# Kernel optimization log

Measured on AMD Instinct MI355X. Metric: run time of the kernel, lower is better.

The kernel has to match this reference:

```python
import jax, jax.numpy as jnp
import numpy as np

# RVQECell configuration (matches init_kwargs)
I_SZ, W_SZ, STAGES, ORDER, DEGREE = 6, 12, 3, 2, 2
BIAS = float(np.pi / 2)
ANC = ORDER - 1                      # ancillas_for_order(order) = order - 1
N = I_SZ + W_SZ + ANC                # 19 qubits
B = 32
INOUT = list(range(I_SZ))            # lanes 0..5
WORK = list(range(I_SZ, I_SZ + W_SZ))  # lanes 6..17
C_CTRL = I_SZ + W_SZ - 1             # controls per neuron = 17


def setup_inputs() -> dict:
    key = jax.random.key(0)
    ks = jax.random.split(key, 9)
    s = 0.1  # small init keeps neuron angles in a well-conditioned range
    psi = jax.random.normal(ks[0], (B, 2 ** N), jnp.float32)
    psi = psi / jnp.linalg.norm(psi, axis=1, keepdims=True)  # normalized kets
    return {
        "batch": psi,
        "w_in1": jax.random.normal(ks[1], (W_SZ, C_CTRL), jnp.float32) * s,
        "w_in2": jax.random.normal(ks[2], (W_SZ, C_CTRL, C_CTRL), jnp.float32) * s,
        "w_u": jax.random.normal(ks[3], (STAGES, W_SZ), jnp.float32) * s,
        "w_k1": jax.random.normal(ks[4], (STAGES, W_SZ, C_CTRL), jnp.float32) * s,
        "w_k2": jax.random.normal(ks[5], (STAGES, W_SZ, C_CTRL, C_CTRL), jnp.float32) * s,
        "w_out1": jax.random.normal(ks[6], (I_SZ, C_CTRL), jnp.float32) * s,
        "w_out2": jax.random.normal(ks[7], (I_SZ, C_CTRL, C_CTRL), jnp.float32) * s,
        "inputs": jax.random.randint(ks[8], (B, I_SZ), 0, 2, dtype=jnp.int32),
    }


def _rot_y(state, lane, alpha):
    # real rotation [[cos a, -sin a], [sin a, cos a]] on qubit `lane`.
    ax = lane + 1  # +1 for batch axis; state shape [B] + [2]*N
    c, s = jnp.cos(alpha), jnp.sin(alpha)
    p0 = jax.lax.index_in_dim(state, 0, ax, keepdims=True)
    p1 = jax.lax.index_in_dim(state, 1, ax, keepdims=True)
    return jnp.concatenate([c * p0 - s * p1, s * p0 + c * p1], axis=ax)


def _neuron(state, outlane, th1, th2):
    # Fast (deterministic RUS) quantum neuron of given ORDER/DEGREE:
    # per control-basis-branch rotation of `outlane` by alpha(x),
    # phi(x) = bias + sum_i th1_i x_i + sum_{i<j} th2_ij x_i x_j (degree 2),
    # alpha = q^(order-1)(phi), q(t) = arctan(tan(t)^2), stable via arctan2.
    controls = [l for l in range(I_SZ + W_SZ) if l != outlane]
    Cn = len(controls)
    x = jnp.arange(2 ** Cn)
    shifts = jnp.arange(Cn - 1, -1, -1)
    bits = ((x[:, None] >> shifts[None, :]) & 1).astype(state.dtype)  # [2^Cn, Cn]
    phi = BIAS + bits @ th1
    if DEGREE >= 2:
        phi = phi + jnp.einsum('xi,ij,xj->x', bits, jnp.triu(th2, 1), bits)
    alpha = phi
    for _ in range(ORDER - 1):
        alpha = jnp.arctan2(jnp.sin(alpha) ** 2, jnp.cos(alpha) ** 2)
    shape = [1] + [2 if l in controls else 1 for l in range(N)]
    return _rot_y(state, outlane, alpha.reshape(shape))


def _bitflip(state_flat, inputs):
    # Vectorized batched BitFlipLayer: X on inout lane i where inputs[b,i]==1,
    # i.e. permute amplitudes by XOR of the flip mask (lane 0 most significant).
    shifts = (N - 1) - jnp.arange(I_SZ)
    f = jnp.sum(inputs.astype(jnp.int32) << shifts[None, :], axis=1)  # [B]
    idx = jnp.arange(2 ** N, dtype=jnp.int32)[None, :] ^ f[:, None]
    return jnp.take_along_axis(state_flat, idx, axis=1)


def reference(batch, w_in1, w_in2, w_u, w_k1, w_k2, w_out1, w_out2, inputs):
    psi = _bitflip(batch, inputs).reshape((B,) + (2,) * N)
    # input layer: one neuron per workspace lane
    for j, out in enumerate(WORK):
        psi = _neuron(psi, out, w_in1[j], w_in2[j])
    # kernel layer: stages x (UnitaryLayer(workspace) + neurons)
    for st in range(STAGES):
        for j, lane in enumerate(WORK):
            psi = _rot_y(psi, lane, w_u[st, j])
        for j, out in enumerate(WORK):
            psi = _neuron(psi, out, w_k1[st, j], w_k2[st, j])
    psi = _bitflip(psi.reshape(B, -1), inputs).reshape((B,) + (2,) * N)
    # output layer: one neuron per inout lane
    for j, out in enumerate(INOUT):
        psi = _neuron(psi, out, w_out1[j], w_out2[j])
    # measurement probabilities over inout lanes: marginal of |amp|^2
    probs = jnp.sum(psi ** 2, axis=tuple(range(1 + I_SZ, 1 + N))).reshape(B, -1)
    return probs, psi.reshape(B, -1)
```

## Files before the change

kernel.cpp:

```cpp
#include <hip/hip_runtime.h>
#include <math.h>


#define BIAS_F 1.57079632679489662f

typedef float v4f __attribute__((ext_vector_type(4)));

__device__ __forceinline__ float4 ntload4(const float* p) {
    v4f v = __builtin_nontemporal_load((const v4f*)p);
    return make_float4(v.x, v.y, v.z, v.w);
}
__device__ __forceinline__ void ntstore4(float* p, float4 f) {
    v4f v = {f.x, f.y, f.z, f.w};
    __builtin_nontemporal_store(v, (v4f*)p);
}

__device__ __forceinline__ int SW(int i) { return i ^ ((i >> 3) & 0x1C); }
__device__ __forceinline__ float4 ldsld4(const float* st, int i) {
    return *(const float4*)&st[SW(i)];
}
__device__ __forceinline__ void ldsst4(float* st, int i, float4 v) {
    *(float4*)&st[SW(i)] = v;
}

__device__ __forceinline__ float2 dec(float v) {
    float t = sqrtf(fmaf(-v, v, 1.0f));
    float c = v >= 0.f ? v : t;
    float s = v >= 0.f ? t : -v;
    return make_float2(c, s);
}
__device__ __forceinline__ float4 dec4(float2 g) {
    float2 u = dec(g.x), w = dec(g.y);
    return make_float4(u.x, u.y, w.x, w.y);
}
#define LD2(p) (*(const float2*)(p))
#define LD4(p) (*(const float4*)(p))

__device__ __forceinline__ void rot4(float4& A, float4& B, float4 e) {
    float ax = A.x, ay = A.y, az = A.z, aw = A.w;
    A.x = e.x * ax - e.y * B.x;  B.x = e.y * ax + e.x * B.x;
    A.y = e.x * ay - e.y * B.y;  B.y = e.y * ay + e.x * B.y;
    A.z = e.z * az - e.w * B.z;  B.z = e.w * az + e.z * B.z;
    A.w = e.z * aw - e.w * B.w;  B.w = e.w * aw + e.z * B.w;
}
__device__ __forceinline__ void rotq(float4& P, float c, float s) {
    float px = P.x, py = P.y;
    P.x = c * px - s * P.z;  P.z = s * px + c * P.z;
    P.y = c * py - s * P.w;  P.w = s * py + c * P.w;
}

__global__ __launch_bounds__(256) void tables_kernel(
    const float* __restrict__ w_in1, const float* __restrict__ w_in2,
    const float* __restrict__ w_k1,  const float* __restrict__ w_k2,
    const float* __restrict__ w_out1, const float* __restrict__ w_out2,
    float* __restrict__ tab)
{
    const int n = blockIdx.y;
    const int hi = blockIdx.x;
    const int tid = threadIdx.x;
    const float* th1;
    const float* th2;
    if (n < 12)      { th1 = w_in1 + n * 17;         th2 = w_in2 + n * 289; }
    else if (n < 48) { th1 = w_k1 + (n - 12) * 17;   th2 = w_k2 + (n - 12) * 289; }
    else             { th1 = w_out1 + (n - 48) * 17; th2 = w_out2 + (n - 48) * 289; }

    float bu[9], bt[8];
#pragma unroll
    for (int i = 0; i < 9; ++i) bu[i] = (float)((hi >> (8 - i)) & 1);
#pragma unroll
    for (int j = 0; j < 8; ++j) bt[j] = (float)((tid >> (7 - j)) & 1);

    float phi = BIAS_F;
#pragma unroll
    for (int i = 0; i < 9; ++i) {
        float acc = th1[i];
#pragma unroll
        for (int j = i + 1; j < 9; ++j) acc += bu[j] * th2[i * 17 + j];
#pragma unroll
        for (int j = 0; j < 8; ++j)     acc += bt[j] * th2[i * 17 + 9 + j];
        phi += bu[i] * acc;
    }
#pragma unroll
    for (int a = 0; a < 8; ++a) {
        float acc = th1[9 + a];
#pragma unroll
        for (int b2 = a + 1; b2 < 8; ++b2) acc += bt[b2] * th2[(9 + a) * 17 + 9 + b2];
        phi += bt[a] * acc;
    }
    float sp, cp;
    sincosf(phi, &sp, &cp);
    float c2 = cp * cp, s2 = sp * sp;
    float d = c2 * c2 + s2 * s2;
    float r = rsqrtf(d);
    r = r * (1.5f - 0.5f * d * r * r);
    float ca = c2 * r, sa = s2 * r;
    tab[(size_t)n * 131072 + ((hi << 8) | tid)] = (ca <= sa) ? ca : -sa;
}

template <int PA, bool NEUR>
__device__ __forceinline__ void pass_hi2(float* l0, float* l1, int t8,
    const float* tA, const float* tB, const float* tC,
    float cA, float sA, float cB, float sB, float cC, float sC)
{
    const int lowb = PA - 4;
    const int low = t8 & ((1 << lowb) - 1);
    const int high = t8 >> lowb;
    const int i0 = (high << (PA + 1)) | (low << 2);
    const int x0 = (high << (PA - 1)) | (low << 1);
    const int oa = 1 << PA, ob = oa >> 1, oc = oa >> 2;
    const int dhi = oa >> 2, dlo = oa >> 3;
    float2 pa0, pa1, pa2, pa3, pb0, pb1, pb2, pb3, pc0, pc1, pc2, pc3;
    if (NEUR) {
        pa0 = LD2(&tA[x0]);       pa1 = LD2(&tA[x0 + dlo]);
        pa2 = LD2(&tA[x0 + dhi]); pa3 = LD2(&tA[x0 + dhi + dlo]);
        pb0 = LD2(&tB[x0]);       pb1 = LD2(&tB[x0 + dlo]);
        pb2 = LD2(&tB[x0 + dhi]); pb3 = LD2(&tB[x0 + dhi + dlo]);
        pc0 = LD2(&tC[x0]);       pc1 = LD2(&tC[x0 + dlo]);
        pc2 = LD2(&tC[x0 + dhi]); pc3 = LD2(&tC[x0 + dhi + dlo]);
    }
#pragma unroll
    for (int s = 0; s < 2; ++s) {
        float* sl = (s == 0) ? l0 : l1;
        float4 Q000 = ldsld4(sl, i0),            Q001 = ldsld4(sl, i0 + oc);
        float4 Q010 = ldsld4(sl, i0 + ob),       Q011 = ldsld4(sl, i0 + ob + oc);
        float4 Q100 = ldsld4(sl, i0 + oa),       Q101 = ldsld4(sl, i0 + oa + oc);
        float4 Q110 = ldsld4(sl, i0 + oa + ob),  Q111 = ldsld4(sl, i0 + oa + ob + oc);
        if (NEUR) {
            {
                float4 e00 = dec4(pa0), e01 = dec4(pa1), e10 = dec4(pa2), e11 = dec4(pa3);
                rot4(Q000, Q100, e00); rot4(Q001, Q101, e01);
                rot4(Q010, Q110, e10); rot4(Q011, Q111, e11);
            }
            {
                float4 e00 = dec4(pb0), e01 = dec4(pb1), e10 = dec4(pb2), e11 = dec4(pb3);
                rot4(Q000, Q010, e00); rot4(Q001, Q011, e01);
                rot4(Q100, Q110, e10); rot4(Q101, Q111, e11);
            }
            {
                float4 e00 = dec4(pc0), e01 = dec4(pc1), e10 = dec4(pc2), e11 = dec4(pc3);
                rot4(Q000, Q001, e00); rot4(Q010, Q011, e01);
                rot4(Q100, Q101, e10); rot4(Q110, Q111, e11);
            }
        } else {
            float4 eA = make_float4(cA, sA, cA, sA);
            rot4(Q000, Q100, eA); rot4(Q001, Q101, eA);
            rot4(Q010, Q110, eA); rot4(Q011, Q111, eA);
            float4 eB = make_float4(cB, sB, cB, sB);
            rot4(Q000, Q010, eB); rot4(Q001, Q011, eB);
            rot4(Q100, Q110, eB); rot4(Q101, Q111, eB);
            float4 eC = make_float4(cC, sC, cC, sC);
            rot4(Q000, Q001, eC); rot4(Q010, Q011, eC);
            rot4(Q100, Q101, eC); rot4(Q110, Q111, eC);
        }
        ldsst4(sl, i0, Q000);            ldsst4(sl, i0 + oc, Q001);
        ldsst4(sl, i0 + ob, Q010);       ldsst4(sl, i0 + ob + oc, Q011);
        ldsst4(sl, i0 + oa, Q100);       ldsst4(sl, i0 + oa + oc, Q101);
        ldsst4(sl, i0 + oa + ob, Q110);  ldsst4(sl, i0 + oa + ob + oc, Q111);
    }
}

template <bool NEUR>
__device__ __forceinline__ void pass_lo2(float* l0, float* l1, int t8,
    const float* tA, const float* tB, const float* tC,
    float cA, float sA, float cB, float sB, float cC, float sC)
{
    const int i0 = t8 << 5, x0 = t8 << 3;
    float4 qa0, qa1, qb0, qb1, qc0, qc1;
    if (NEUR) {
        qa0 = LD4(&tA[x0]); qa1 = LD4(&tA[x0 + 4]);
        qb0 = LD4(&tB[x0]); qb1 = LD4(&tB[x0 + 4]);
        qc0 = LD4(&tC[x0]); qc1 = LD4(&tC[x0 + 4]);
    }
#pragma unroll
    for (int s = 0; s < 2; ++s) {
        float* sl = (s == 0) ? l0 : l1;
        float4 Q0 = ldsld4(sl, i0),      Q1 = ldsld4(sl, i0 + 4);
        float4 Q2 = ldsld4(sl, i0 + 8),  Q3 = ldsld4(sl, i0 + 12);
        float4 Q4 = ldsld4(sl, i0 + 16), Q5 = ldsld4(sl, i0 + 20);
        float4 Q6 = ldsld4(sl, i0 + 24), Q7 = ldsld4(sl, i0 + 28);
        if (NEUR) {
            rot4(Q0, Q2, dec4(make_float2(qa0.x, qa0.y)));
            rot4(Q1, Q3, dec4(make_float2(qa0.z, qa0.w)));
            rot4(Q4, Q6, dec4(make_float2(qa1.x, qa1.y)));
            rot4(Q5, Q7, dec4(make_float2(qa1.z, qa1.w)));
            rot4(Q0, Q1, dec4(make_float2(qb0.x, qb0.y)));
            rot4(Q2, Q3, dec4(make_float2(qb0.z, qb0.w)));
            rot4(Q4, Q5, dec4(make_float2(qb1.x, qb1.y)));
            rot4(Q6, Q7, dec4(make_float2(qb1.z, qb1.w)));
            { float2 d = dec(qc0.x); rotq(Q0, d.x, d.y); }
            { float2 d = dec(qc0.y); rotq(Q1, d.x, d.y); }
            { float2 d = dec(qc0.z); rotq(Q2, d.x, d.y); }
            { float2 d = dec(qc0.w); rotq(Q3, d.x, d.y); }
            { float2 d = dec(qc1.x); rotq(Q4, d.x, d.y); }
            { float2 d = dec(qc1.y); rotq(Q5, d.x, d.y); }
            { float2 d = dec(qc1.z); rotq(Q6, d.x, d.y); }
            { float2 d = dec(qc1.w); rotq(Q7, d.x, d.y); }
        } else {
            float4 eA = make_float4(cA, sA, cA, sA);
            rot4(Q0, Q2, eA); rot4(Q1, Q3, eA); rot4(Q4, Q6, eA); rot4(Q5, Q7, eA);
            float4 eB = make_float4(cB, sB, cB, sB);
            rot4(Q0, Q1, eB); rot4(Q2, Q3, eB); rot4(Q4, Q5, eB); rot4(Q6, Q7, eB);
            rotq(Q0, cC, sC); rotq(Q1, cC, sC); rotq(Q2, cC, sC); rotq(Q3, cC, sC);
            rotq(Q4, cC, sC); rotq(Q5, cC, sC); rotq(Q6, cC, sC); rotq(Q7, cC, sC);
        }
        ldsst4(sl, i0, Q0);      ldsst4(sl, i0 + 4, Q1);
        ldsst4(sl, i0 + 8, Q2);  ldsst4(sl, i0 + 12, Q3);
        ldsst4(sl, i0 + 16, Q4); ldsst4(sl, i0 + 20, Q5);
        ldsst4(sl, i0 + 24, Q6); ldsst4(sl, i0 + 28, Q7);
    }
}

__global__ __launch_bounds__(256, 2) void main_kernel(
    const float* __restrict__ batch, const float* __restrict__ w_u,
    const int* __restrict__ inputs, const float* __restrict__ tab,
    float* __restrict__ psi, float* __restrict__ probs)
{
    __shared__ __align__(16) float lds[2][8192];
    const int t8 = threadIdx.x;
    const int blk = blockIdx.x;
    const int xcd = blk & 7;
    const int vt = (xcd << 3) | ((blk >> 3) & 7);
    const int pair = blk >> 6;

    if (blk == 0) {
        float4 z = make_float4(0.f, 0.f, 0.f, 0.f);
        *(float4*)&probs[t8 * 8] = z;
        *(float4*)&probs[t8 * 8 + 4] = z;
    }

    int bb[2], uu[2];
#pragma unroll
    for (int s = 0; s < 2; ++s) {
        int b = pair * 2 + s;
        int fb = 0;
#pragma unroll
        for (int i = 0; i < 6; ++i) fb |= (inputs[b * 6 + i] & 1) << (5 - i);
        bb[s] = b; uu[s] = vt ^ fb;
        const float* src = batch + ((size_t)b << 19) + ((size_t)uu[s] << 13);
#pragma unroll
        for (int k = 0; k < 8; ++k) {
            int i4 = (k * 256 + t8) * 4;
            float4 v = ntload4(&src[i4]);
            *(float4*)&lds[s][SW(i4)] = v;
        }
    }
    float* l0 = lds[0];
    float* l1 = lds[1];

    const float* tb = tab + (vt << 11);
#define TN(j) (tb + (size_t)(j) * 131072)
#define BAR __syncthreads()
    BAR;
    pass_hi2<12, true>(l0, l1, t8, TN(0), TN(1), TN(2), 0,0,0,0,0,0);  BAR;
    pass_hi2<9,  true>(l0, l1, t8, TN(3), TN(4), TN(5), 0,0,0,0,0,0);  BAR;
    pass_hi2<6,  true>(l0, l1, t8, TN(6), TN(7), TN(8), 0,0,0,0,0,0);  BAR;
    pass_lo2<true>(l0, l1, t8, TN(9), TN(10), TN(11), 0,0,0,0,0,0);    BAR;

#pragma unroll 1
    for (int st2 = 0; st2 < 3; ++st2) {
        const float* wu = w_u + st2 * 12;
        float c0, s0, c1, s1, c2, s2;
        sincosf(wu[0], &s0, &c0); sincosf(wu[1], &s1, &c1); sincosf(wu[2], &s2, &c2);
        pass_hi2<12, false>(l0, l1, t8, 0,0,0, c0,s0, c1,s1, c2,s2);   BAR;
        sincosf(wu[3], &s0, &c0); sincosf(wu[4], &s1, &c1); sincosf(wu[5], &s2, &c2);
        pass_hi2<9, false>(l0, l1, t8, 0,0,0, c0,s0, c1,s1, c2,s2);    BAR;
        sincosf(wu[6], &s0, &c0); sincosf(wu[7], &s1, &c1); sincosf(wu[8], &s2, &c2);
        pass_hi2<6, false>(l0, l1, t8, 0,0,0, c0,s0, c1,s1, c2,s2);    BAR;
        sincosf(wu[9], &s0, &c0); sincosf(wu[10], &s1, &c1); sincosf(wu[11], &s2, &c2);
        pass_lo2<false>(l0, l1, t8, 0,0,0, c0,s0, c1,s1, c2,s2);       BAR;

        const int nb = 12 + st2 * 12;
        pass_hi2<12, true>(l0, l1, t8, TN(nb+0), TN(nb+1), TN(nb+2), 0,0,0,0,0,0); BAR;
        pass_hi2<9,  true>(l0, l1, t8, TN(nb+3), TN(nb+4), TN(nb+5), 0,0,0,0,0,0); BAR;
        pass_hi2<6,  true>(l0, l1, t8, TN(nb+6), TN(nb+7), TN(nb+8), 0,0,0,0,0,0); BAR;
        pass_lo2<true>(l0, l1, t8, TN(nb+9), TN(nb+10), TN(nb+11), 0,0,0,0,0,0);   BAR;
    }
#undef TN
#undef BAR

#pragma unroll
    for (int s = 0; s < 2; ++s) {
        float* dst = psi + ((size_t)bb[s] << 19) + ((size_t)uu[s] << 13);
#pragma unroll
        for (int k = 0; k < 8; ++k) {
            int i4 = (k * 256 + t8) * 4;
            float4 v = *(const float4*)&lds[s][SW(i4)];
            ntstore4(&dst[i4], v);
        }
    }
}

__global__ __launch_bounds__(256, 2) void out_kernel(
    const float* __restrict__ tab, float* __restrict__ psi,
    float* __restrict__ probs)
{
    __shared__ float ts[16384];
    const int tid = threadIdx.x;
    const int b = blockIdx.x >> 5;
    const int col = ((blockIdx.x & 31) << 8) | tid;
    float* base = psi + ((size_t)b << 19) + col;
    float a[64];
#pragma unroll
    for (int k = 0; k < 64; ++k)
        a[k] = __builtin_nontemporal_load(&base[(size_t)k << 13]);
    const int w12 = col >> 1;
#pragma unroll
    for (int j = 0; j < 6; ++j) {
        const float* tj = tab + (size_t)(48 + j) * 131072 + w12;
        const int q = 5 - j;
#pragma unroll
        for (int m = 0; m < 32; ++m) {
            int k0 = ((m >> q) << (q + 1)) | (m & ((1 << q) - 1));
            int k1 = k0 | (1 << q);
            float2 e = dec(tj[(size_t)m << 12]);
            float a0 = a[k0], a1 = a[k1];
            a[k0] = e.x * a0 - e.y * a1;
            a[k1] = e.y * a0 + e.x * a1;
        }
    }
#pragma unroll
    for (int k = 0; k < 64; ++k)
        __builtin_nontemporal_store(a[k], &base[(size_t)k << 13]);

    const int jx = tid & 63;
#pragma unroll
    for (int k = 0; k < 64; ++k) ts[tid * 64 + (k ^ jx)] = a[k] * a[k];
    __syncthreads();
    const int k = tid & 63, seg = tid >> 6;
    float p = 0.f;
#pragma unroll
    for (int j = 0; j < 64; ++j) p += ts[(seg * 64 + j) * 64 + (k ^ j)];
    atomicAdd(&probs[b * 64 + k], p);
}

extern "C" void kernel_launch(void* const* d_in, const int* in_sizes, int n_in,
                              void* d_out, int out_size, void* d_ws, size_t ws_size,
                              hipStream_t stream)
{
    const float* batch  = (const float*)d_in[0];
    const float* w_in1  = (const float*)d_in[1];
    const float* w_in2  = (const float*)d_in[2];
    const float* w_u    = (const float*)d_in[3];
    const float* w_k1   = (const float*)d_in[4];
    const float* w_k2   = (const float*)d_in[5];
    const float* w_out1 = (const float*)d_in[6];
    const float* w_out2 = (const float*)d_in[7];
    const int*   inputs = (const int*)d_in[8];
    float* probs = (float*)d_out;
    float* psi   = (float*)d_out + 2048;
    float* tab   = (float*)d_ws;

    tables_kernel<<<dim3(512, 54), 256, 0, stream>>>(w_in1, w_in2, w_k1, w_k2,
                                                     w_out1, w_out2, tab);
    main_kernel<<<1024, 256, 0, stream>>>(batch, w_u, inputs, tab, psi, probs);
    out_kernel<<<1024, 256, 0, stream>>>(tab, psi, probs);
}
```

Before: 390.2 us.

## Split batch slots across 512-thread blocks and stage out_kernel I/O through LDS

The main kernel now runs with 512 threads per block. Each half of the block handles one of the two batch slices that a single thread used to process in sequence, so per-thread work and register pressure are halved and more waves are resident to hide latency. The output kernel now loads and stores psi as coalesced float4 rows staged through swizzled shared memory instead of strided scalar accesses. It also preloads each stage's 32 table values before the rotations and squares amplitudes during the probability reduction. The cost is extra shared-memory traffic and barriers in the output kernel, and larger blocks that must synchronise more threads at every pass barrier.

```diff
diff --git a/kernel.cpp b/kernel.cpp
--- a/kernel.cpp
+++ b/kernel.cpp
@@ -98,7 +98,7 @@
 }
 
 template <int PA, bool NEUR>
-__device__ __forceinline__ void pass_hi2(float* l0, float* l1, int t8,
+__device__ __forceinline__ void pass_hi(float* sl, int t8,
     const float* tA, const float* tB, const float* tC,
     float cA, float sA, float cB, float sB, float cC, float sC)
 {
@@ -109,58 +109,37 @@
     const int x0 = (high << (PA - 1)) | (low << 1);
     const int oa = 1 << PA, ob = oa >> 1, oc = oa >> 2;
     const int dhi = oa >> 2, dlo = oa >> 3;
-    float2 pa0, pa1, pa2, pa3, pb0, pb1, pb2, pb3, pc0, pc1, pc2, pc3;
+    float4 ea00, ea01, ea10, ea11, eb00, eb01, eb10, eb11, ec00, ec01, ec10, ec11;
     if (NEUR) {
-        pa0 = LD2(&tA[x0]);       pa1 = LD2(&tA[x0 + dlo]);
-        pa2 = LD2(&tA[x0 + dhi]); pa3 = LD2(&tA[x0 + dhi + dlo]);
-        pb0 = LD2(&tB[x0]);       pb1 = LD2(&tB[x0 + dlo]);
-        pb2 = LD2(&tB[x0 + dhi]); pb3 = LD2(&tB[x0 + dhi + dlo]);
-        pc0 = LD2(&tC[x0]);       pc1 = LD2(&tC[x0 + dlo]);
-        pc2 = LD2(&tC[x0 + dhi]); pc3 = LD2(&tC[x0 + dhi + dlo]);
-    }
-#pragma unroll
-    for (int s = 0; s < 2; ++s) {
-        float* sl = (s == 0) ? l0 : l1;
-        float4 Q000 = ldsld4(sl, i0),            Q001 = ldsld4(sl, i0 + oc);
-        float4 Q010 = ldsld4(sl, i0 + ob),       Q011 = ldsld4(sl, i0 + ob + oc);
-        float4 Q100 = ldsld4(sl, i0 + oa),       Q101 = ldsld4(sl, i0 + oa + oc);
-        float4 Q110 = ldsld4(sl, i0 + oa + ob),  Q111 = ldsld4(sl, i0 + oa + ob + oc);
-        if (NEUR) {
-            {
-                float4 e00 = dec4(pa0), e01 = dec4(pa1), e10 = dec4(pa2), e11 = dec4(pa3);
-                rot4(Q000, Q100, e00); rot4(Q001, Q101, e01);
-                rot4(Q010, Q110, e10); rot4(Q011, Q111, e11);
-            }
-            {
-                float4 e00 = dec4(pb0), e01 = dec4(pb1), e10 = dec4(pb2), e11 = dec4(pb3);
-                rot4(Q000, Q010, e00); rot4(Q001, Q011, e01);
-                rot4(Q100, Q110, e10); rot4(Q101, Q111, e11);
-            }
-            {
-                float4 e00 = dec4(pc0), e01 = dec4(pc1), e10 = dec4(pc2), e11 = dec4(pc3);
-                rot4(Q000, Q001, e00); rot4(Q010, Q011, e01);
-                rot4(Q100, Q101, e10); rot4(Q110, Q111, e11);
-            }
-        } else {
-            float4 eA = make_float4(cA, sA, cA, sA);
-            rot4(Q000, Q100, eA); rot4(Q001, Q101, eA);
-            rot4(Q010, Q110, eA); rot4(Q011, Q111, eA);
-            float4 eB = make_float4(cB, sB, cB, sB);
-            rot4(Q000, Q010, eB); rot4(Q001, Q011, eB);
-            rot4(Q100, Q110, eB); rot4(Q101, Q111, eB);
-            float4 eC = make_float4(cC, sC, cC, sC);
-            rot4(Q000, Q001, eC); rot4(Q010, Q011, eC);
-            rot4(Q100, Q101, eC); rot4(Q110, Q111, eC);
-        }
-        ldsst4(sl, i0, Q000);            ldsst4(sl, i0 + oc, Q001);
-        ldsst4(sl, i0 + ob, Q010);       ldsst4(sl, i0 + ob + oc, Q011);
-        ldsst4(sl, i0 + oa, Q100);       ldsst4(sl, i0 + oa + oc, Q101);
-        ldsst4(sl, i0 + oa + ob, Q110);  ldsst4(sl, i0 + oa + ob + oc, Q111);
-    }
+        ea00 = dec4(LD2(&tA[x0]));        ea01 = dec4(LD2(&tA[x0 + dlo]));
+        ea10 = dec4(LD2(&tA[x0 + dhi]));  ea11 = dec4(LD2(&tA[x0 + dhi + dlo]));
+        eb00 = dec4(LD2(&tB[x0]));        eb01 = dec4(LD2(&tB[x0 + dlo]));
+        eb10 = dec4(LD2(&tB[x0 + dhi]));  eb11 = dec4(LD2(&tB[x0 + dhi + dlo]));
+        ec00 = dec4(LD2(&tC[x0]));        ec01 = dec4(LD2(&tC[x0 + dlo]));
+        ec10 = dec4(LD2(&tC[x0 + dhi]));  ec11 = dec4(LD2(&tC[x0 + dhi + dlo]));
+    } else {
+        ea00 = ea01 = ea10 = ea11 = make_float4(cA, sA, cA, sA);
+        eb00 = eb01 = eb10 = eb11 = make_float4(cB, sB, cB, sB);
+        ec00 = ec01 = ec10 = ec11 = make_float4(cC, sC, cC, sC);
+    }
+    float4 Q000 = ldsld4(sl, i0),            Q001 = ldsld4(sl, i0 + oc);
+    float4 Q010 = ldsld4(sl, i0 + ob),       Q011 = ldsld4(sl, i0 + ob + oc);
+    float4 Q100 = ldsld4(sl, i0 + oa),       Q101 = ldsld4(sl, i0 + oa + oc);
+    float4 Q110 = ldsld4(sl, i0 + oa + ob),  Q111 = ldsld4(sl, i0 + oa + ob + oc);
+    rot4(Q000, Q100, ea00); rot4(Q001, Q101, ea01);
+    rot4(Q010, Q110, ea10); rot4(Q011, Q111, ea11);
+    rot4(Q000, Q010, eb00); rot4(Q001, Q011, eb01);
+    rot4(Q100, Q110, eb10); rot4(Q101, Q111, eb11);
+    rot4(Q000, Q001, ec00); rot4(Q010, Q011, ec01);
+    rot4(Q100, Q101, ec10); rot4(Q110, Q111, ec11);
+    ldsst4(sl, i0, Q000);            ldsst4(sl, i0 + oc, Q001);
+    ldsst4(sl, i0 + ob, Q010);       ldsst4(sl, i0 + ob + oc, Q011);
+    ldsst4(sl, i0 + oa, Q100);       ldsst4(sl, i0 + oa + oc, Q101);
+    ldsst4(sl, i0 + oa + ob, Q110);  ldsst4(sl, i0 + oa + ob + oc, Q111);
 }
 
 template <bool NEUR>
-__device__ __forceinline__ void pass_lo2(float* l0, float* l1, int t8,
+__device__ __forceinline__ void pass_lo(float* sl, int t8,
     const float* tA, const float* tB, const float* tC,
     float cA, float sA, float cB, float sB, float cC, float sC)
 {
@@ -171,52 +150,50 @@
         qb0 = LD4(&tB[x0]); qb1 = LD4(&tB[x0 + 4]);
         qc0 = LD4(&tC[x0]); qc1 = LD4(&tC[x0 + 4]);
     }
-#pragma unroll
-    for (int s = 0; s < 2; ++s) {
-        float* sl = (s == 0) ? l0 : l1;
-        float4 Q0 = ldsld4(sl, i0),      Q1 = ldsld4(sl, i0 + 4);
-        float4 Q2 = ldsld4(sl, i0 + 8),  Q3 = ldsld4(sl, i0 + 12);
-        float4 Q4 = ldsld4(sl, i0 + 16), Q5 = ldsld4(sl, i0 + 20);
-        float4 Q6 = ldsld4(sl, i0 + 24), Q7 = ldsld4(sl, i0 + 28);
-        if (NEUR) {
-            rot4(Q0, Q2, dec4(make_float2(qa0.x, qa0.y)));
-            rot4(Q1, Q3, dec4(make_float2(qa0.z, qa0.w)));
-            rot4(Q4, Q6, dec4(make_float2(qa1.x, qa1.y)));
-            rot4(Q5, Q7, dec4(make_float2(qa1.z, qa1.w)));
-            rot4(Q0, Q1, dec4(make_float2(qb0.x, qb0.y)));
-            rot4(Q2, Q3, dec4(make_float2(qb0.z, qb0.w)));
-            rot4(Q4, Q5, dec4(make_float2(qb1.x, qb1.y)));
-            rot4(Q6, Q7, dec4(make_float2(qb1.z, qb1.w)));
-            { float2 d = dec(qc0.x); rotq(Q0, d.x, d.y); }
-            { float2 d = dec(qc0.y); rotq(Q1, d.x, d.y); }
-            { float2 d = dec(qc0.z); rotq(Q2, d.x, d.y); }
-            { float2 d = dec(qc0.w); rotq(Q3, d.x, d.y); }
-            { float2 d = dec(qc1.x); rotq(Q4, d.x, d.y); }
-            { float2 d = dec(qc1.y); rotq(Q5, d.x, d.y); }
-            { float2 d = dec(qc1.z); rotq(Q6, d.x, d.y); }
-            { float2 d = dec(qc1.w); rotq(Q7, d.x, d.y); }
-        } else {
-            float4 eA = make_float4(cA, sA, cA, sA);
-            rot4(Q0, Q2, eA); rot4(Q1, Q3, eA); rot4(Q4, Q6, eA); rot4(Q5, Q7, eA);
-            float4 eB = make_float4(cB, sB, cB, sB);
-            rot4(Q0, Q1, eB); rot4(Q2, Q3, eB); rot4(Q4, Q5, eB); rot4(Q6, Q7, eB);
-            rotq(Q0, cC, sC); rotq(Q1, cC, sC); rotq(Q2, cC, sC); rotq(Q3, cC, sC);
-            rotq(Q4, cC, sC); rotq(Q5, cC, sC); rotq(Q6, cC, sC); rotq(Q7, cC, sC);
-        }
-        ldsst4(sl, i0, Q0);      ldsst4(sl, i0 + 4, Q1);
-        ldsst4(sl, i0 + 8, Q2);  ldsst4(sl, i0 + 12, Q3);
-        ldsst4(sl, i0 + 16, Q4); ldsst4(sl, i0 + 20, Q5);
-        ldsst4(sl, i0 + 24, Q6); ldsst4(sl, i0 + 28, Q7);
-    }
-}
-
-__global__ __launch_bounds__(256, 2) void main_kernel(
+    float4 Q0 = ldsld4(sl, i0),      Q1 = ldsld4(sl, i0 + 4);
+    float4 Q2 = ldsld4(sl, i0 + 8),  Q3 = ldsld4(sl, i0 + 12);
+    float4 Q4 = ldsld4(sl, i0 + 16), Q5 = ldsld4(sl, i0 + 20);
+    float4 Q6 = ldsld4(sl, i0 + 24), Q7 = ldsld4(sl, i0 + 28);
+    if (NEUR) {
+        rot4(Q0, Q2, dec4(make_float2(qa0.x, qa0.y)));
+        rot4(Q1, Q3, dec4(make_float2(qa0.z, qa0.w)));
+        rot4(Q4, Q6, dec4(make_float2(qa1.x, qa1.y)));
+        rot4(Q5, Q7, dec4(make_float2(qa1.z, qa1.w)));
+        rot4(Q0, Q1, dec4(make_float2(qb0.x, qb0.y)));
+        rot4(Q2, Q3, dec4(make_float2(qb0.z, qb0.w)));
+        rot4(Q4, Q5, dec4(make_float2(qb1.x, qb1.y)));
+        rot4(Q6, Q7, dec4(make_float2(qb1.z, qb1.w)));
+        { float2 d = dec(qc0.x); rotq(Q0, d.x, d.y); }
+        { float2 d = dec(qc0.y); rotq(Q1, d.x, d.y); }
+        { float2 d = dec(qc0.z); rotq(Q2, d.x, d.y); }
+        { float2 d = dec(qc0.w); rotq(Q3, d.x, d.y); }
+        { float2 d = dec(qc1.x); rotq(Q4, d.x, d.y); }
+        { float2 d = dec(qc1.y); rotq(Q5, d.x, d.y); }
+        { float2 d = dec(qc1.z); rotq(Q6, d.x, d.y); }
+        { float2 d = dec(qc1.w); rotq(Q7, d.x, d.y); }
+    } else {
+        float4 eA = make_float4(cA, sA, cA, sA);
+        rot4(Q0, Q2, eA); rot4(Q1, Q3, eA); rot4(Q4, Q6, eA); rot4(Q5, Q7, eA);
+        float4 eB = make_float4(cB, sB, cB, sB);
+        rot4(Q0, Q1, eB); rot4(Q2, Q3, eB); rot4(Q4, Q5, eB); rot4(Q6, Q7, eB);
+        rotq(Q0, cC, sC); rotq(Q1, cC, sC); rotq(Q2, cC, sC); rotq(Q3, cC, sC);
+        rotq(Q4, cC, sC); rotq(Q5, cC, sC); rotq(Q6, cC, sC); rotq(Q7, cC, sC);
+    }
+    ldsst4(sl, i0, Q0);      ldsst4(sl, i0 + 4, Q1);
+    ldsst4(sl, i0 + 8, Q2);  ldsst4(sl, i0 + 12, Q3);
+    ldsst4(sl, i0 + 16, Q4); ldsst4(sl, i0 + 20, Q5);
+    ldsst4(sl, i0 + 24, Q6); ldsst4(sl, i0 + 28, Q7);
+}
+
+__global__ __launch_bounds__(512, 4) void main_kernel(
     const float* __restrict__ batch, const float* __restrict__ w_u,
     const int* __restrict__ inputs, const float* __restrict__ tab,
     float* __restrict__ psi, float* __restrict__ probs)
 {
     __shared__ __align__(16) float lds[2][8192];
-    const int t8 = threadIdx.x;
+    const int tid = threadIdx.x;
+    const int t8 = tid & 255;
+    const int slot = tid >> 8;
     const int blk = blockIdx.x;
     const int xcd = blk & 7;
     const int vt = (xcd << 3) | ((blk >> 3) & 7);
@@ -224,67 +201,62 @@
 
     if (blk == 0) {
         float4 z = make_float4(0.f, 0.f, 0.f, 0.f);
-        *(float4*)&probs[t8 * 8] = z;
-        *(float4*)&probs[t8 * 8 + 4] = z;
-    }
-
-    int bb[2], uu[2];
-#pragma unroll
-    for (int s = 0; s < 2; ++s) {
-        int b = pair * 2 + s;
-        int fb = 0;
-#pragma unroll
-        for (int i = 0; i < 6; ++i) fb |= (inputs[b * 6 + i] & 1) << (5 - i);
-        bb[s] = b; uu[s] = vt ^ fb;
-        const float* src = batch + ((size_t)b << 19) + ((size_t)uu[s] << 13);
+        *(float4*)&probs[tid * 4] = z;
+    }
+
+    const int b = pair * 2 + slot;
+    int fb = 0;
+#pragma unroll
+    for (int i = 0; i < 6; ++i) fb |= (inputs[b * 6 + i] & 1) << (5 - i);
+    const int u = vt ^ fb;
+    float* sl = lds[slot];
+    {
+        const float* src = batch + ((size_t)b << 19) + ((size_t)u << 13);
 #pragma unroll
         for (int k = 0; k < 8; ++k) {
             int i4 = (k * 256 + t8) * 4;
             float4 v = ntload4(&src[i4]);
-            *(float4*)&lds[s][SW(i4)] = v;
+            *(float4*)&sl[SW(i4)] = v;
         }
     }
-    float* l0 = lds[0];
-    float* l1 = lds[1];
 
     const float* tb = tab + (vt << 11);
 #define TN(j) (tb + (size_t)(j) * 131072)
 #define BAR __syncthreads()
     BAR;
-    pass_hi2<12, true>(l0, l1, t8, TN(0), TN(1), TN(2), 0,0,0,0,0,0);  BAR;
-    pass_hi2<9,  true>(l0, l1, t8, TN(3), TN(4), TN(5), 0,0,0,0,0,0);  BAR;
-    pass_hi2<6,  true>(l0, l1, t8, TN(6), TN(7), TN(8), 0,0,0,0,0,0);  BAR;
-    pass_lo2<true>(l0, l1, t8, TN(9), TN(10), TN(11), 0,0,0,0,0,0);    BAR;
+    pass_hi<12, true>(sl, t8, TN(0), TN(1), TN(2), 0,0,0,0,0,0);  BAR;
+    pass_hi<9,  true>(sl, t8, TN(3), TN(4), TN(5), 0,0,0,0,0,0);  BAR;
+    pass_hi<6,  true>(sl, t8, TN(6), TN(7), TN(8), 0,0,0,0,0,0);  BAR;
+    pass_lo<true>(sl, t8, TN(9), TN(10), TN(11), 0,0,0,0,0,0);    BAR;
 
 #pragma unroll 1
     for (int st2 = 0; st2 < 3; ++st2) {
         const float* wu = w_u + st2 * 12;
         float c0, s0, c1, s1, c2, s2;
         sincosf(wu[0], &s0, &c0); sincosf(wu[1], &s1, &c1); sincosf(wu[2], &s2, &c2);
-        pass_hi2<12, false>(l0, l1, t8, 0,0,0, c0,s0, c1,s1, c2,s2);   BAR;
+        pass_hi<12, false>(sl, t8, 0,0,0, c0,s0, c1,s1, c2,s2);   BAR;
         sincosf(wu[3], &s0, &c0); sincosf(wu[4], &s1, &c1); sincosf(wu[5], &s2, &c2);
-        pass_hi2<9, false>(l0, l1, t8, 0,0,0, c0,s0, c1,s1, c2,s2);    BAR;
+        pass_hi<9, false>(sl, t8, 0,0,0, c0,s0, c1,s1, c2,s2);    BAR;
         sincosf(wu[6], &s0, &c0); sincosf(wu[7], &s1, &c1); sincosf(wu[8], &s2, &c2);
-        pass_hi2<6, false>(l0, l1, t8, 0,0,0, c0,s0, c1,s1, c2,s2);    BAR;
+        pass_hi<6, false>(sl, t8, 0,0,0, c0,s0, c1,s1, c2,s2);    BAR;
         sincosf(wu[9], &s0, &c0); sincosf(wu[10], &s1, &c1); sincosf(wu[11], &s2, &c2);
-        pass_lo2<false>(l0, l1, t8, 0,0,0, c0,s0, c1,s1, c2,s2);       BAR;
+        pass_lo<false>(sl, t8, 0,0,0, c0,s0, c1,s1, c2,s2);       BAR;
 
         const int nb = 12 + st2 * 12;
-        pass_hi2<12, true>(l0, l1, t8, TN(nb+0), TN(nb+1), TN(nb+2), 0,0,0,0,0,0); BAR;
-        pass_hi2<9,  true>(l0, l1, t8, TN(nb+3), TN(nb+4), TN(nb+5), 0,0,0,0,0,0); BAR;
-        pass_hi2<6,  true>(l0, l1, t8, TN(nb+6), TN(nb+7), TN(nb+8), 0,0,0,0,0,0); BAR;
-        pass_lo2<true>(l0, l1, t8, TN(nb+9), TN(nb+10), TN(nb+11), 0,0,0,0,0,0);   BAR;
+        pass_hi<12, true>(sl, t8, TN(nb+0), TN(nb+1), TN(nb+2), 0,0,0,0,0,0); BAR;
+        pass_hi<9,  true>(sl, t8, TN(nb+3), TN(nb+4), TN(nb+5), 0,0,0,0,0,0); BAR;
+        pass_hi<6,  true>(sl, t8, TN(nb+6), TN(nb+7), TN(nb+8), 0,0,0,0,0,0); BAR;
+        pass_lo<true>(sl, t8, TN(nb+9), TN(nb+10), TN(nb+11), 0,0,0,0,0,0);   BAR;
     }
 #undef TN
 #undef BAR
 
-#pragma unroll
-    for (int s = 0; s < 2; ++s) {
-        float* dst = psi + ((size_t)bb[s] << 19) + ((size_t)uu[s] << 13);
+    {
+        float* dst = psi + ((size_t)b << 19) + ((size_t)u << 13);
 #pragma unroll
         for (int k = 0; k < 8; ++k) {
             int i4 = (k * 256 + t8) * 4;
-            float4 v = *(const float4*)&lds[s][SW(i4)];
+            float4 v = *(const float4*)&sl[SW(i4)];
             ntstore4(&dst[i4], v);
         }
     }
@@ -294,43 +266,66 @@
     const float* __restrict__ tab, float* __restrict__ psi,
     float* __restrict__ probs)
 {
-    __shared__ float ts[16384];
+    __shared__ __align__(16) float ts[16384];
     const int tid = threadIdx.x;
+    const int lane = tid & 63;
+    const int wv = tid >> 6;
     const int b = blockIdx.x >> 5;
-    const int col = ((blockIdx.x & 31) << 8) | tid;
-    float* base = psi + ((size_t)b << 19) + col;
+    const int c0 = (blockIdx.x & 31) << 8;
+    float* gbase = psi + ((size_t)b << 19) + c0;
+
+#pragma unroll
+    for (int i = 0; i < 16; ++i) {
+        int k = wv * 16 + i;
+        float4 v = ntload4(&gbase[((size_t)k << 13) + lane * 4]);
+        int f4 = lane ^ (k & 15);
+        *(float4*)&ts[k * 256 + f4 * 4] = v;
+    }
+    __syncthreads();
+
     float a[64];
 #pragma unroll
-    for (int k = 0; k < 64; ++k)
-        a[k] = __builtin_nontemporal_load(&base[(size_t)k << 13]);
-    const int w12 = col >> 1;
-#pragma unroll
-    for (int j = 0; j < 6; ++j) {
-        const float* tj = tab + (size_t)(48 + j) * 131072 + w12;
-        const int q = 5 - j;
-#pragma unroll
-        for (int m = 0; m < 32; ++m) {
-            int k0 = ((m >> q) << (q + 1)) | (m & ((1 << q) - 1));
-            int k1 = k0 | (1 << q);
-            float2 e = dec(tj[(size_t)m << 12]);
-            float a0 = a[k0], a1 = a[k1];
-            a[k0] = e.x * a0 - e.y * a1;
-            a[k1] = e.y * a0 + e.x * a1;
-        }
-    }
-#pragma unroll
-    for (int k = 0; k < 64; ++k)
-        __builtin_nontemporal_store(a[k], &base[(size_t)k << 13]);
-
-    const int jx = tid & 63;
-#pragma unroll
-    for (int k = 0; k < 64; ++k) ts[tid * 64 + (k ^ jx)] = a[k] * a[k];
+    for (int k = 0; k < 64; ++k) a[k] = ts[k * 256 + (tid ^ ((k & 15) << 2))];
+    const int w12 = (c0 | tid) >> 1;
+
+#define OSTAGE(J) { \
+    const float* tj = tab + (size_t)(48 + (J)) * 131072 + w12; \
+    float ev[32]; \
+    _Pragma("unroll") \
+    for (int m = 0; m < 32; ++m) ev[m] = tj[(size_t)m << 12]; \
+    _Pragma("unroll") \
+    for (int m = 0; m < 32; ++m) { \
+        const int q = 5 - (J); \
+        const int k0 = ((m >> q) << (q + 1)) | (m & ((1 << q) - 1)); \
+        const int k1 = k0 | (1 << q); \
+        float2 e = dec(ev[m]); \
+        float A0 = a[k0], A1 = a[k1]; \
+        a[k0] = e.x * A0 - e.y * A1; \
+        a[k1] = e.y * A0 + e.x * A1; } }
+    OSTAGE(0) OSTAGE(1) OSTAGE(2) OSTAGE(3) OSTAGE(4) OSTAGE(5)
+#undef OSTAGE
+
+#pragma unroll
+    for (int k = 0; k < 64; ++k) ts[k * 256 + (tid ^ ((k & 15) << 2))] = a[k];
     __syncthreads();
-    const int k = tid & 63, seg = tid >> 6;
+
+#pragma unroll
+    for (int i = 0; i < 16; ++i) {
+        int k = wv * 16 + i;
+        int f4 = lane ^ (k & 15);
+        float4 v = *(const float4*)&ts[k * 256 + f4 * 4];
+        ntstore4(&gbase[((size_t)k << 13) + lane * 4], v);
+    }
+
+    const int k6 = tid & 63, seg = tid >> 6;
     float p = 0.f;
 #pragma unroll
-    for (int j = 0; j < 64; ++j) p += ts[(seg * 64 + j) * 64 + (k ^ j)];
-    atomicAdd(&probs[b * 64 + k], p);
+    for (int j = 0; j < 64; ++j) {
+        int c = seg * 64 + ((j + k6) & 63);
+        float v = ts[k6 * 256 + (c ^ ((k6 & 15) << 2))];
+        p += v * v;
+    }
+    atomicAdd(&probs[b * 64 + k6], p);
 }
 
 extern "C" void kernel_launch(void* const* d_in, const int* in_sizes, int n_in,
@@ -352,6 +347,6 @@
 
     tables_kernel<<<dim3(512, 54), 256, 0, stream>>>(w_in1, w_in2, w_k1, w_k2,
                                                      w_out1, w_out2, tab);
-    main_kernel<<<1024, 256, 0, stream>>>(batch, w_u, inputs, tab, psi, probs);
+    main_kernel<<<1024, 512, 0, stream>>>(batch, w_u, inputs, tab, psi, probs);
     out_kernel<<<1024, 256, 0, stream>>>(tab, psi, probs);
 }
```

After: 465.5 us. 19.3% more time.
